# Kernel optimization log

Measured on AMD Instinct MI355X. Metric: run time of the kernel, lower is better.

## Reference

```python
import jax, jax.numpy as jnp
import numpy as np

B, H, W = 16, 32, 32
N = H * W
C_SEARCH, C_XCORR = 256, 64
C = C_SEARCH + C_XCORR          # phi_in_channels = gcn_in_channels
PHI_H = 64
GC_HID, GC_OUT = 128, 1
K_PTS = 48                       # keypoints per image
BN_EPS = 1e-5


def _build_coords_pair():
    # 8-neighbourhood pairs (distance^2 in {1,2}), exactly gen_8neigh_coords_pair
    idx = np.arange(N).reshape(H, W)
    ys, xs = np.meshgrid(np.arange(H), np.arange(W), indexing='ij')
    pairs8 = []
    for dy in (-1, 0, 1):
        for dx in (-1, 0, 1):
            if dy == 0 and dx == 0:
                continue
            ny, nx = ys + dy, xs + dx
            m = (ny >= 0) & (ny < H) & (nx >= 0) & (nx < W)
            pairs8.append(np.stack([idx[ys[m], xs[m]], idx[ny[m], nx[m]]], axis=1))
    pairs8 = np.concatenate(pairs8, 0)  # [7812, 2]
    # keypoint permutation pairs; keypoints on even coords -> disjoint from 8-neigh
    even = np.arange(0, H, 2)
    grid_idx = (even[:, None] * W + even[None, :]).reshape(-1)
    rng = np.random.default_rng(0)
    out = []
    for _ in range(B):
        kp = rng.choice(grid_idx, size=K_PTS, replace=False)
        a, b = np.meshgrid(kp, kp, indexing='ij')
        m = a != b
        kpairs = np.stack([a[m], b[m]], axis=1)  # K*(K-1) ordered pairs
        out.append(np.concatenate([kpairs, pairs8], 0))
    return np.stack(out, 0).astype(np.int32)  # [B, E, 2]


def setup_inputs() -> dict:
    key = jax.random.key(0)
    ks = jax.random.split(key, 10)
    u = lambda k, shape, s: jax.random.uniform(k, shape, jnp.float32, -s, s)
    inp = {
        'search_feature': jax.random.normal(ks[0], (B, C_SEARCH, H, W), jnp.float32),
        'xcorr_map': jax.random.normal(ks[1], (B, C_XCORR, H, W), jnp.float32),
        'coords_pair': jnp.asarray(_build_coords_pair()),
        # phi: Linear(C, PHI_H) + BN + ReLU, then Linear(PHI_H, 1) + Sigmoid
        'phi_w1': u(ks[2], (C, PHI_H), 1.0 / np.sqrt(C)),
        'phi_b1': u(ks[3], (PHI_H,), 1.0 / np.sqrt(C)),
        'bn_gamma': jnp.ones((PHI_H,), jnp.float32),
        'bn_beta': jnp.zeros((PHI_H,), jnp.float32),
        'phi_w2': u(ks[4], (PHI_H, 1), 1.0 / np.sqrt(PHI_H)),
        'phi_b2': u(ks[5], (1,), 1.0 / np.sqrt(PHI_H)),
        # GCN weights, torch init: uniform(-1/sqrt(out), 1/sqrt(out))
        'gc1_w': u(ks[6], (C, GC_HID), 1.0 / np.sqrt(GC_HID)),
        'gc2_w': u(ks[7], (GC_HID, GC_OUT), 1.0 / np.sqrt(GC_OUT)),
    }
    return inp


def reference(search_feature, xcorr_map, coords_pair, phi_w1, phi_b1,
              bn_gamma, bn_beta, phi_w2, phi_b2, gc1_w, gc2_w):
    # catted feature flattened: [B, C, N] (row-major h*W+w, matches torch view)
    feat = jnp.concatenate([search_feature, xcorr_map], axis=1).reshape(B, C, N)

    def per_image(f, pairs):  # f: [C, N], pairs: [E, 2]
        diff = jnp.abs(f[:, pairs[:, 0]] - f[:, pairs[:, 1]]).T  # [E, C]
        h = diff @ phi_w1 + phi_b1                                # [E, PHI_H]
        mu = jnp.mean(h, axis=0)
        var = jnp.var(h, axis=0)  # biased, as torch BN training mode
        h = (h - mu) / jnp.sqrt(var + BN_EPS) * bn_gamma + bn_beta
        h = jax.nn.relu(h)
        edge = jax.nn.sigmoid(h @ phi_w2 + phi_b2)[:, 0]          # [E]
        adj = jnp.zeros((N, N), jnp.float32).at[pairs[:, 0], pairs[:, 1]].set(edge)
        return adj

    adj = jax.vmap(per_image)(feat, coords_pair)  # [B, N, N]

    node_feat = feat.transpose(0, 2, 1)  # [B, N, C] (gcn_process_feat_xcorr=True)
    h = jax.nn.leaky_relu(jnp.einsum('bnm,bmd->bnd', adj, node_feat @ gc1_w), 0.2)
    mask = jax.nn.sigmoid(jnp.einsum('bnm,bmd->bnd', adj, h @ gc2_w))  # [B, N, 1]
    return mask[:, :, 0].reshape(B, 1, H, W)
```

## Files before the change

### kernel.cpp

```cpp
#include <hip/hip_runtime.h>
#include <hip/hip_bf16.h>
#include <hip/hip_fp16.h>

#define BB 16
#define NN 1024
#define CS 256
#define CX 64
#define CC 320
#define PH 64
#define GH 128
#define ELLW 64
#define NENG 7812
#define ROWP 324
#define RSTR 164
#define NKPH 1128
#define NGU  3906
#define NUD  5034

typedef __hip_bfloat16 bf16;
typedef __attribute__((ext_vector_type(8))) __bf16 bfrag;
typedef __attribute__((ext_vector_type(4))) float v4f;

__device__ __forceinline__ void tri_decode(int m, int& a, int& y) {
    float s = sqrtf((float)(9025 - 8 * m));
    int aa = (int)((95.0f - s) * 0.5f);
    if (aa > 0 && 47 * aa - (aa * (aa - 1)) / 2 > m) --aa;
    while (47 * (aa + 1) - ((aa + 1) * aa) / 2 <= m) ++aa;
    a = aa;
    y = aa + 1 + (m - (47 * aa - (aa * (aa - 1)) / 2));
}

__global__ __launch_bounds__(256) void k_prep_transpose(
    const float* __restrict__ search, const float* __restrict__ xcorr,
    float* __restrict__ featT,
    const float* __restrict__ w1, const float* __restrict__ gc1w,
    __bf16* __restrict__ whi, __bf16* __restrict__ wlo,
    __bf16* __restrict__ gwhi, __bf16* __restrict__ gwlo,
    int* __restrict__ cnt, float* __restrict__ Ssum, float* __restrict__ S2sum)
{
    __shared__ float tile[32][33];
    int blk = blockIdx.x;
    int tid = threadIdx.x;
    if (blk < BB * 320) {
        int b   = blk % BB;
        int rem = blk / BB;
        int ct  = rem >> 5;
        int ntl = rem & 31;
        int cl = tid >> 5, nl = tid & 31;
        const float* sb = search + (size_t)b * CS * NN;
        const float* xb = xcorr + (size_t)b * CX * NN;
        #pragma unroll
        for (int f = 0; f < 4; ++f) {
            int c = ct * 32 + cl + f * 8;
            int n = ntl * 32 + nl;
            float v = (c < CS) ? sb[(size_t)c * NN + n] : xb[(size_t)(c - CS) * NN + n];
            tile[cl + f * 8][nl] = v;
        }
        __syncthreads();
        #pragma unroll
        for (int f = 0; f < 4; ++f) {
            int nr = cl + f * 8;
            int cc = nl;
            featT[((size_t)b * NN + ntl * 32 + nr) * CC + ct * 32 + cc] = tile[cc][nr];
        }
    } else {
        int idx = (blk - BB * 320) * 256 + tid;
        if (idx < 10 * 4 * 64 * 8) {
            int j    = idx & 7;
            int lane = (idx >> 3) & 63;
            int nt   = (idx >> 9) & 3;
            int ks   = idx >> 11;
            int k = ks * 32 + (lane >> 4) * 8 + j;
            int n = nt * 16 + (lane & 15);
            float w = w1[k * PH + n];
            __bf16 h = (__bf16)w;
            whi[idx] = h;
            wlo[idx] = (__bf16)(w - (float)h);
        }
        if (idx < 10 * 8 * 64 * 8) {
            int j    = idx & 7;
            int lane = (idx >> 3) & 63;
            int nt   = (idx >> 9) & 7;
            int ks   = idx >> 12;
            int k = ks * 32 + (lane >> 4) * 8 + j;
            int n = nt * 16 + (lane & 15);
            float w = gc1w[k * GH + n];
            __bf16 h = (__bf16)w;
            gwhi[idx] = h;
            gwlo[idx] = (__bf16)(w - (float)h);
        }
        if (idx < BB * NN) cnt[idx] = 0;
        if (idx < BB * PH) { Ssum[idx] = 0.f; S2sum[idx] = 0.f; }
    }
}

__global__ __launch_bounds__(512, 1) void k_edge(
    const float* __restrict__ featT, const int* __restrict__ pairs,
    const uint4* __restrict__ wglob, const float* __restrict__ b1,
    bf16* __restrict__ hstore, float* __restrict__ Ssum,
    float* __restrict__ S2sum, int E, int EKP)
{
    __shared__ ushort Wsh[40960];
    __shared__ float RowsBuf[16000];
    __shared__ int kpn[48];

    int t = threadIdx.x;
    int wave = t >> 6, lane = t & 63;
    int q = lane >> 4, r = lane & 15;
    int b = blockIdx.x % BB;
    int s = blockIdx.x / BB;

    if (t < 48) kpn[t] = pairs[((size_t)b * E + t * 47) * 2];

    {
        uint4* dst = (uint4*)Wsh;
        #pragma unroll
        for (int k = 0; k < 10; ++k)
            dst[t + k * 512] = wglob[t + k * 512];
    }
    const bfrag* WH = (const bfrag*)Wsh;
    const bfrag* WL = (const bfrag*)(Wsh + 20480);

    float b1v[4];
    #pragma unroll
    for (int nt = 0; nt < 4; ++nt) b1v[nt] = b1[nt * 16 + r];
    float ps[4], ps2[4];
    #pragma unroll
    for (int nt = 0; nt < 4; ++nt) { ps[nt] = 0.f; ps2[nt] = 0.f; }

    const int dyT[4] = {-1,-1,-1, 0};
    const int dxT[4] = {-1, 0, 1,-1};
    const int pfT4[4] = {0, 961, 1953, 2914};

    int d = wave >> 1;
    int p = wave & 1;
    int dy = dyT[d], dx = dxT[d];
    int y0 = dy < 0 ? 1 : 0;
    int x0 = dx < 0 ? 1 : 0;
    int ww = (dx == 0) ? 32 : 31;
    int pfF = pfT4[d];
    int y = 2 * s + p;

    const float* rowI[2];
    const float* rowJ[2];
    #pragma unroll
    for (int mt = 0; mt < 2; ++mt) {
        int x  = (mt << 4) + r;
        int lr = 1 + p;
        int ni = lr * 32 + x;
        int xj = x + dx; xj = xj < 0 ? 0 : (xj > 31 ? 31 : xj);
        int nj = (lr + dy) * 32 + xj;
        rowI[mt] = &RowsBuf[ni * RSTR + q * 8];
        rowJ[mt] = &RowsBuf[nj * RSTR + q * 8];
    }

    v4f acc[2][4];
    #pragma unroll
    for (int mt = 0; mt < 2; ++mt)
        #pragma unroll
        for (int nt = 0; nt < 4; ++nt) acc[mt][nt] = (v4f)0.f;

    #pragma unroll
    for (int ph = 0; ph < 2; ++ph) {
        __syncthreads();
        const int ch0 = ph * 160;
        for (int uu = t; uu < 96 * 40; uu += 512) {
            int node = uu / 40, c4 = uu - node * 40;
            int gy = 2 * s - 1 + (node >> 5);
            if (gy >= 0) {
                int gn = gy * 32 + (node & 31);
                float4 v = *(const float4*)&featT[((size_t)b * NN + gn) * CC
                                                  + ch0 + c4 * 4];
                *(float4*)&RowsBuf[node * RSTR + c4 * 4] = v;
            }
        }
        __syncthreads();

        const int ksBeg = ph * 5;
        #pragma unroll
        for (int ks = ksBeg; ks < ksBeg + 5; ++ks) {
            int lc = ks * 32 - ch0;
            #pragma unroll
            for (int mt = 0; mt < 2; ++mt) {
                float4 fi0 = *(const float4*)(rowI[mt] + lc);
                float4 fi1 = *(const float4*)(rowI[mt] + lc + 4);
                float4 fj0 = *(const float4*)(rowJ[mt] + lc);
                float4 fj1 = *(const float4*)(rowJ[mt] + lc + 4);
                float df[8];
                df[0] = fabsf(fi0.x - fj0.x); df[1] = fabsf(fi0.y - fj0.y);
                df[2] = fabsf(fi0.z - fj0.z); df[3] = fabsf(fi0.w - fj0.w);
                df[4] = fabsf(fi1.x - fj1.x); df[5] = fabsf(fi1.y - fj1.y);
                df[6] = fabsf(fi1.z - fj1.z); df[7] = fabsf(fi1.w - fj1.w);

                bfrag ah, al;
                #pragma unroll
                for (int kk = 0; kk < 8; ++kk) {
                    __bf16 h = (__bf16)df[kk];
                    ah[kk] = h;
                    al[kk] = (__bf16)(df[kk] - (float)h);
                }
                #pragma unroll
                for (int nt = 0; nt < 4; ++nt) {
                    bfrag bh = WH[((ks * 4 + nt) << 6) + lane];
                    bfrag bl = WL[((ks * 4 + nt) << 6) + lane];
                    acc[mt][nt] = __builtin_amdgcn_mfma_f32_16x16x32_bf16(
                        ah, bh, acc[mt][nt], 0, 0, 0);
                    acc[mt][nt] = __builtin_amdgcn_mfma_f32_16x16x32_bf16(
                        ah, bl, acc[mt][nt], 0, 0, 0);
                    acc[mt][nt] = __builtin_amdgcn_mfma_f32_16x16x32_bf16(
                        al, bh, acc[mt][nt], 0, 0, 0);
                }
            }
        }
    }

    __syncthreads();
    {
        const float4* src = (const float4*)featT;
        #pragma unroll
        for (int k = 0; k < 8; ++k) {
            int idx = t + k * 512;
            if (idx < 48 * 80) {
                int slot = idx / 80, c4 = idx - slot * 80;
                float4 v = src[((size_t)b * NN + kpn[slot]) * 80 + c4];
                *(float4*)&RowsBuf[slot * ROWP + c4 * 4] = v;
            }
        }
    }

    #pragma unroll
    for (int mt = 0; mt < 2; ++mt) {
        #pragma unroll
        for (int reg = 0; reg < 4; ++reg) {
            int xi = (mt << 4) + q * 4 + reg;
            int y2 = y + dy, x2 = xi + dx;
            bool valid = ((unsigned)y2 < 32u) && ((unsigned)x2 < 32u);
            if (valid) {
                int e1 = EKP + pfF + (y - y0) * ww + (xi - x0);
                bf16* h1 = hstore + ((size_t)b * E + e1) * PH + r;
                #pragma unroll
                for (int nt = 0; nt < 4; ++nt) {
                    float v = acc[mt][nt][reg] + b1v[nt];
                    h1[nt * 16] = __float2bfloat16(v);
                    ps[nt] += v;
                    ps2[nt] = fmaf(v, v, ps2[nt]);
                }
            }
        }
    }

    __syncthreads();

    int u = s + 16 * wave;
    if (u < 71) {
        int mA = u * 16 + r;
        if (mA >= NKPH) mA = NKPH - 1;
        int aI, yI;
        tri_decode(mA, aI, yI);
        const float* rI = &RowsBuf[aI * ROWP + q * 8];
        const float* rJ = &RowsBuf[yI * ROWP + q * 8];

        v4f acc2[4];
        #pragma unroll
        for (int nt = 0; nt < 4; ++nt) acc2[nt] = (v4f)0.f;

        #pragma unroll
        for (int ks = 0; ks < 10; ++ks) {
            float4 fi0 = *(const float4*)(rI + ks * 32);
            float4 fi1 = *(const float4*)(rI + ks * 32 + 4);
            float4 fj0 = *(const float4*)(rJ + ks * 32);
            float4 fj1 = *(const float4*)(rJ + ks * 32 + 4);
            float df[8];
            df[0] = fabsf(fi0.x - fj0.x); df[1] = fabsf(fi0.y - fj0.y);
            df[2] = fabsf(fi0.z - fj0.z); df[3] = fabsf(fi0.w - fj0.w);
            df[4] = fabsf(fi1.x - fj1.x); df[5] = fabsf(fi1.y - fj1.y);
            df[6] = fabsf(fi1.z - fj1.z); df[7] = fabsf(fi1.w - fj1.w);

            bfrag ah, al;
            #pragma unroll
            for (int kk = 0; kk < 8; ++kk) {
                __bf16 h = (__bf16)df[kk];
                ah[kk] = h;
                al[kk] = (__bf16)(df[kk] - (float)h);
            }
            #pragma unroll
            for (int nt = 0; nt < 4; ++nt) {
                bfrag bh = WH[((ks * 4 + nt) << 6) + lane];
                bfrag bl = WL[((ks * 4 + nt) << 6) + lane];
                acc2[nt] = __builtin_amdgcn_mfma_f32_16x16x32_bf16(ah, bh, acc2[nt], 0, 0, 0);
                acc2[nt] = __builtin_amdgcn_mfma_f32_16x16x32_bf16(ah, bl, acc2[nt], 0, 0, 0);
                acc2[nt] = __builtin_amdgcn_mfma_f32_16x16x32_bf16(al, bh, acc2[nt], 0, 0, 0);
            }
        }

        #pragma unroll
        for (int reg = 0; reg < 4; ++reg) {
            int mC = u * 16 + q * 4 + reg;
            if (mC < NKPH) {
                int a, yk;
                tri_decode(mC, a, yk);
                int e1 = a * 47 + yk - 1;
                bf16* h1 = hstore + ((size_t)b * E + e1) * PH + r;
                #pragma unroll
                for (int nt = 0; nt < 4; ++nt) {
                    float v = acc2[nt][reg] + b1v[nt];
                    h1[nt * 16] = __float2bfloat16(v);
                    ps[nt] += v;
                    ps2[nt] = fmaf(v, v, ps2[nt]);
                }
            }
        }
    }

    __syncthreads();
    float* sS  = RowsBuf;
    float* sS2 = RowsBuf + PH;
    if (t < PH) { sS[t] = 0.f; sS2[t] = 0.f; }
    __syncthreads();
    #pragma unroll
    for (int nt = 0; nt < 4; ++nt) {
        float p1 = ps[nt]  + __shfl_xor(ps[nt], 16, 64);
        p1 += __shfl_xor(p1, 32, 64);
        float p2 = ps2[nt] + __shfl_xor(ps2[nt], 16, 64);
        p2 += __shfl_xor(p2, 32, 64);
        if (lane < 16) {
            atomicAdd(&sS[nt * 16 + r],  2.0f * p1);
            atomicAdd(&sS2[nt * 16 + r], 2.0f * p2);
        }
    }
    __syncthreads();
    if (t < PH) {
        atomicAdd(&Ssum[b * PH + t],  sS[t]);
        atomicAdd(&S2sum[b * PH + t], sS2[t]);
    }
}

__global__ __launch_bounds__(256, 2) void k_val_gc1(
    const float* __restrict__ featT, const __bf16* __restrict__ gwhi,
    const __bf16* __restrict__ gwlo, __half* __restrict__ g1,
    const bf16* __restrict__ hstore, const float* __restrict__ Ssum,
    const float* __restrict__ S2sum, const float* __restrict__ gamma,
    const float* __restrict__ beta, const float* __restrict__ w2,
    const float* __restrict__ b2, const int* __restrict__ pairs,
    int* __restrict__ cnt, int* __restrict__ ecol, float* __restrict__ eval_,
    int E, int EKP, int nGC)
{
    __shared__ ushort WG[40960];

    int t = threadIdx.x;
    if ((int)blockIdx.x < nGC) {
        int b = blockIdx.x % BB;
        int rem = blockIdx.x / BB;
        int half = rem & 1;
        int m0 = b * NN + (rem >> 1) * 64;

        {
            uint4* dst = (uint4*)WG;
            const uint4* sh = (const uint4*)gwhi;
            const uint4* sl = (const uint4*)gwlo;
            #pragma unroll
            for (int k = 0; k < 10; ++k) {
                int u = t + k * 256;
                int chunk = u >> 6, v = u & 63;
                int ks = chunk >> 2, ntp = chunk & 3;
                int src = (ks * 8 + half * 4 + ntp) * 64 + v;
                dst[u]        = sh[src];
                dst[2560 + u] = sl[src];
            }
        }

        int wave = t >> 6, lane = t & 63;
        int q = lane >> 4, r = lane & 15;
        const float* fp = featT + (size_t)(m0 + wave * 16 + r) * CC + q * 8;

        float fa[2][8];
        auto LOADA = [&](int ks, int buf) {
            const float4* p = (const float4*)(fp + ks * 32);
            *(float4*)&fa[buf][0] = p[0];
            *(float4*)&fa[buf][4] = p[1];
        };

        v4f acc[4];
        #pragma unroll
        for (int nt = 0; nt < 4; ++nt) acc[nt] = (v4f)0.f;

        LOADA(0, 0);
        __syncthreads();

        const bfrag* WGH = (const bfrag*)WG;
        const bfrag* WGL = (const bfrag*)(WG + 20480);

        #pragma unroll
        for (int ks = 0; ks < 10; ++ks) {
            int cur = ks & 1;
            if (ks < 9) LOADA(ks + 1, cur ^ 1);
            bfrag ah, al;
            #pragma unroll
            for (int kk = 0; kk < 8; ++kk) {
                float d = fa[cur][kk];
                __bf16 h = (__bf16)d;
                ah[kk] = h;
                al[kk] = (__bf16)(d - (float)h);
            }
            #pragma unroll
            for (int nt = 0; nt < 4; ++nt) {
                bfrag bh = WGH[((ks * 4 + nt) << 6) + lane];
                bfrag bl = WGL[((ks * 4 + nt) << 6) + lane];
                acc[nt] = __builtin_amdgcn_mfma_f32_16x16x32_bf16(ah, bh, acc[nt], 0, 0, 0);
                acc[nt] = __builtin_amdgcn_mfma_f32_16x16x32_bf16(ah, bl, acc[nt], 0, 0, 0);
                acc[nt] = __builtin_amdgcn_mfma_f32_16x16x32_bf16(al, bh, acc[nt], 0, 0, 0);
            }
        }
        #pragma unroll
        for (int nt = 0; nt < 4; ++nt) {
            #pragma unroll
            for (int reg = 0; reg < 4; ++reg) {
                int m = m0 + wave * 16 + q * 4 + reg;
                g1[(size_t)m * GH + (half * 4 + nt) * 16 + r] =
                    __float2half(acc[nt][reg]);
            }
        }
    } else {
        float* ca = (float*)WG;
        float* cb = ca + PH;
        int* kpl = (int*)(cb + PH);
        int blk = blockIdx.x - nGC;
        int b = blk % BB;
        int u = (blk / BB) * 256 + t;
        if (t < PH) {
            int l = t;
            float mu = Ssum[b * PH + l] / E;
            float var = S2sum[b * PH + l] / E - mu * mu;
            float A = rsqrtf(var + 1e-5f) * gamma[l];
            ca[l] = A;
            cb[l] = beta[l] - mu * A;
        }
        if (t < 48) kpl[t] = pairs[((size_t)b * E + t * 47) * 2];
        __syncthreads();
        if (u >= NUD) return;

        int i, j, hrow;
        if (u < NKPH) {
            int a, yk;
            tri_decode(u, a, yk);
            i = kpl[a]; j = kpl[yk];
            hrow = a * 47 + yk - 1;
        } else {
            int up = u - NKPH;
            int pf, ww, y0, x0, dy, dx;
            if (up < 961)       { pf = 0;    ww = 31; y0 = 1; x0 = 1; dy = -1; dx = -1; }
            else if (up < 1953) { pf = 961;  ww = 32; y0 = 1; x0 = 0; dy = -1; dx = 0;  }
            else if (up < 2914) { pf = 1953; ww = 31; y0 = 1; x0 = 0; dy = -1; dx = 1;  }
            else                { pf = 2914; ww = 31; y0 = 0; x0 = 1; dy = 0;  dx = -1; }
            int rel = up - pf;
            int yR = rel / ww, xC = rel - yR * ww;
            int yy = yR + y0, xi = xC + x0;
            i = yy * 32 + xi;
            j = (yy + dy) * 32 + (xi + dx);
            hrow = EKP + up;
        }

        const bfrag* hp = (const bfrag*)(hstore + ((size_t)b * E + hrow) * PH);
        float acc = 0.f;
        #pragma unroll
        for (int l8 = 0; l8 < 8; ++l8) {
            bfrag hv = hp[l8];
            #pragma unroll
            for (int c = 0; c < 8; ++c) {
                int l = l8 * 8 + c;
                float x = fmaf((float)hv[c], ca[l], cb[l]);
                x = x > 0.f ? x : 0.f;
                acc = fmaf(x, w2[l], acc);
            }
        }
        float edge = 1.f / (1.f + __expf(-(acc + b2[0])));
        int ri = b * NN + i;
        int rj = b * NN + j;
        int s1 = atomicAdd(&cnt[ri], 1);
        if (s1 < ELLW) {
            ecol[ri * ELLW + s1]  = j;
            eval_[ri * ELLW + s1] = edge;
        }
        int s2 = atomicAdd(&cnt[rj], 1);
        if (s2 < ELLW) {
            ecol[rj * ELLW + s2]  = i;
            eval_[rj * ELLW + s2] = edge;
        }
    }
}

__global__ __launch_bounds__(256) void k_spmm1(
    const __half* __restrict__ g1, const int* __restrict__ cnt,
    const int* __restrict__ ecol, const float* __restrict__ eval_,
    const float* __restrict__ w2g, float* __restrict__ g2)
{
    int tid = threadIdx.x & 63;
    int node = blockIdx.x * 4 + (threadIdx.x >> 6);
    int base = node & ~(NN - 1);
    float wa = w2g[2 * tid], wb = w2g[2 * tid + 1];
    int c = cnt[node];
    const int* ec = ecol + (size_t)node * ELLW;
    const float* ev = eval_ + (size_t)node * ELLW;
    const __half2* g1v = (const __half2*)g1;
    float aa = 0.f, ab = 0.f;
    int s = 0;
    for (; s + 4 <= c; s += 4) {
        int j0 = ec[s], j1 = ec[s + 1], j2 = ec[s + 2], j3 = ec[s + 3];
        float v0 = ev[s], v1 = ev[s + 1], v2 = ev[s + 2], v3 = ev[s + 3];
        __half2 u0 = g1v[((size_t)(base + j0)) * 64 + tid];
        __half2 u1 = g1v[((size_t)(base + j1)) * 64 + tid];
        __half2 u2 = g1v[((size_t)(base + j2)) * 64 + tid];
        __half2 u3 = g1v[((size_t)(base + j3)) * 64 + tid];
        aa = fmaf(v0, __low2float(u0), aa); ab = fmaf(v0, __high2float(u0), ab);
        aa = fmaf(v1, __low2float(u1), aa); ab = fmaf(v1, __high2float(u1), ab);
        aa = fmaf(v2, __low2float(u2), aa); ab = fmaf(v2, __high2float(u2), ab);
        aa = fmaf(v3, __low2float(u3), aa); ab = fmaf(v3, __high2float(u3), ab);
    }
    for (; s < c; ++s) {
        __half2 u = g1v[((size_t)(base + ec[s])) * 64 + tid];
        float v = ev[s];
        aa = fmaf(v, __low2float(u), aa); ab = fmaf(v, __high2float(u), ab);
    }
    float h1a = aa > 0.f ? aa : 0.2f * aa;
    float h1b = ab > 0.f ? ab : 0.2f * ab;
    float p = h1a * wa + h1b * wb;
    #pragma unroll
    for (int off = 32; off >= 1; off >>= 1) p += __shfl_down(p, off, 64);
    if (tid == 0) g2[node] = p;
}

__global__ __launch_bounds__(256) void k_spmm2(
    const float* __restrict__ g2, const int* __restrict__ cnt,
    const int* __restrict__ ecol, const float* __restrict__ eval_,
    float* __restrict__ out)
{
    int lane = threadIdx.x & 63;
    int node = blockIdx.x * 4 + (threadIdx.x >> 6);
    int base = node & ~(NN - 1);
    int c = cnt[node];
    float p = 0.f;
    if (lane < c) {
        int j = ecol[(size_t)node * ELLW + lane];
        p = eval_[(size_t)node * ELLW + lane] * g2[base + j];
    }
    #pragma unroll
    for (int off = 32; off >= 1; off >>= 1) p += __shfl_down(p, off, 64);
    if (lane == 0) out[node] = 1.f / (1.f + __expf(-p));
}

extern "C" void kernel_launch(void* const* d_in, const int* in_sizes, int n_in,
                              void* d_out, int out_size, void* d_ws, size_t ws_size,
                              hipStream_t stream)
{
    const float* search = (const float*)d_in[0];
    const float* xcorr  = (const float*)d_in[1];
    const int*   pairs  = (const int*)d_in[2];
    const float* w1     = (const float*)d_in[3];
    const float* b1     = (const float*)d_in[4];
    const float* gamma  = (const float*)d_in[5];
    const float* beta   = (const float*)d_in[6];
    const float* w2     = (const float*)d_in[7];
    const float* b2     = (const float*)d_in[8];
    const float* gc1w   = (const float*)d_in[9];
    const float* gc2w   = (const float*)d_in[10];
    float* out = (float*)d_out;

    int E   = in_sizes[2] / (BB * 2);
    int EKP = E - NENG;
    int nbU  = (NUD + 255) / 256;
    int nGC  = BB * 32;

    char* ws = (char*)d_ws;
    size_t off = 0;
    auto alloc = [&](size_t bytes) {
        size_t o = off;
        off += (bytes + 255) & ~(size_t)255;
        return o;
    };
    __bf16* whi   = (__bf16*)(ws + alloc(10 * 4 * 64 * 8 * 2));
    __bf16* wlo   = (__bf16*)(ws + alloc(10 * 4 * 64 * 8 * 2));
    __bf16* gwhi  = (__bf16*)(ws + alloc(10 * 8 * 64 * 8 * 2));
    __bf16* gwlo  = (__bf16*)(ws + alloc(10 * 8 * 64 * 8 * 2));
    float* featT  = (float*)(ws + alloc((size_t)BB * NN * CC * 4));
    bf16*  hstore = (bf16*)(ws + alloc((size_t)BB * E * PH * 2));
    float* Ssum   = (float*)(ws + alloc(BB * PH * 4));
    float* S2sum  = (float*)(ws + alloc(BB * PH * 4));
    int*   cnt    = (int*)(ws + alloc(BB * NN * 4));
    int*   ecol   = (int*)(ws + alloc((size_t)BB * NN * ELLW * 4));
    float* eval_  = (float*)(ws + alloc((size_t)BB * NN * ELLW * 4));
    __half* g1    = (__half*)(ws + alloc((size_t)BB * NN * GH * 2));
    float* g2     = (float*)(ws + alloc(BB * NN * 4));
    (void)ws_size; (void)n_in; (void)out_size;

    k_prep_transpose<<<dim3(BB * 320 + 160), dim3(256), 0, stream>>>(
        search, xcorr, featT, w1, gc1w, whi, wlo, gwhi, gwlo, cnt, Ssum, S2sum);
    k_edge<<<dim3(BB * 16), dim3(512), 0, stream>>>(featT, pairs,
                                                    (const uint4*)whi, b1,
                                                    hstore, Ssum, S2sum,
                                                    E, EKP);
    k_val_gc1<<<dim3(nGC + BB * nbU), dim3(256), 0, stream>>>(
        featT, gwhi, gwlo, g1, hstore, Ssum, S2sum, gamma, beta, w2, b2,
        pairs, cnt, ecol, eval_, E, EKP, nGC);
    k_spmm1<<<dim3(BB * NN / 4), dim3(256), 0, stream>>>(g1, cnt, ecol, eval_,
                                                         gc2w, g2);
    k_spmm2<<<dim3(BB * NN / 4), dim3(256), 0, stream>>>(g2, cnt, ecol, eval_, out);
}
```

Measured before the change: 148.2 us.

## Split edge kernel into one-row blocks and read weights directly from global

The edge-MLP kernel now launches twice as many blocks of 256 threads, each handling a single image row instead of two, with four waves covering the four neighbour directions. The per-block copy of the bf16 weight fragments into shared memory is removed, and fragments are loaded from global memory (through cache) during the MFMA loop. Together these cut LDS use so two blocks can share a CU and give more parallelism. The cost is reloading the 3-row halo per block, which is now redundant across neighbouring blocks, plus weight fetches that go to L1/L2 instead of LDS.

```diff
diff --git a/kernel.cpp b/kernel.cpp
--- a/kernel.cpp
+++ b/kernel.cpp
@@ -94,32 +94,25 @@
     }
 }
 
-__global__ __launch_bounds__(512, 1) void k_edge(
+__global__ __launch_bounds__(256, 2) void k_edge(
     const float* __restrict__ featT, const int* __restrict__ pairs,
-    const uint4* __restrict__ wglob, const float* __restrict__ b1,
+    const __bf16* __restrict__ wglob, const float* __restrict__ b1,
     bf16* __restrict__ hstore, float* __restrict__ Ssum,
     float* __restrict__ S2sum, int E, int EKP)
 {
-    __shared__ ushort Wsh[40960];
-    __shared__ float RowsBuf[16000];
+    __shared__ float RowsBuf[15552];
     __shared__ int kpn[48];
 
     int t = threadIdx.x;
     int wave = t >> 6, lane = t & 63;
     int q = lane >> 4, r = lane & 15;
     int b = blockIdx.x % BB;
-    int s = blockIdx.x / BB;
+    int y = blockIdx.x / BB;
 
     if (t < 48) kpn[t] = pairs[((size_t)b * E + t * 47) * 2];
 
-    {
-        uint4* dst = (uint4*)Wsh;
-        #pragma unroll
-        for (int k = 0; k < 10; ++k)
-            dst[t + k * 512] = wglob[t + k * 512];
-    }
-    const bfrag* WH = (const bfrag*)Wsh;
-    const bfrag* WL = (const bfrag*)(Wsh + 20480);
+    const bfrag* WH = (const bfrag*)wglob;
+    const bfrag* WL = WH + 2560;
 
     float b1v[4];
     #pragma unroll
@@ -132,24 +125,21 @@
     const int dxT[4] = {-1, 0, 1,-1};
     const int pfT4[4] = {0, 961, 1953, 2914};
 
-    int d = wave >> 1;
-    int p = wave & 1;
+    int d = wave;
     int dy = dyT[d], dx = dxT[d];
     int y0 = dy < 0 ? 1 : 0;
     int x0 = dx < 0 ? 1 : 0;
     int ww = (dx == 0) ? 32 : 31;
     int pfF = pfT4[d];
-    int y = 2 * s + p;
 
     const float* rowI[2];
     const float* rowJ[2];
     #pragma unroll
     for (int mt = 0; mt < 2; ++mt) {
         int x  = (mt << 4) + r;
-        int lr = 1 + p;
-        int ni = lr * 32 + x;
+        int ni = 32 + x;
         int xj = x + dx; xj = xj < 0 ? 0 : (xj > 31 ? 31 : xj);
-        int nj = (lr + dy) * 32 + xj;
+        int nj = (1 + dy) * 32 + xj;
         rowI[mt] = &RowsBuf[ni * RSTR + q * 8];
         rowJ[mt] = &RowsBuf[nj * RSTR + q * 8];
     }
@@ -164,9 +154,11 @@
     for (int ph = 0; ph < 2; ++ph) {
         __syncthreads();
         const int ch0 = ph * 160;
-        for (int uu = t; uu < 96 * 40; uu += 512) {
+        #pragma unroll
+        for (int k = 0; k < 10; ++k) {
+            int uu = t + k * 256;
             int node = uu / 40, c4 = uu - node * 40;
-            int gy = 2 * s - 1 + (node >> 5);
+            int gy = y - 1 + (node >> 5);
             if (gy >= 0) {
                 int gn = gy * 32 + (node & 31);
                 float4 v = *(const float4*)&featT[((size_t)b * NN + gn) * CC
@@ -218,13 +210,11 @@
     {
         const float4* src = (const float4*)featT;
         #pragma unroll
-        for (int k = 0; k < 8; ++k) {
-            int idx = t + k * 512;
-            if (idx < 48 * 80) {
-                int slot = idx / 80, c4 = idx - slot * 80;
-                float4 v = src[((size_t)b * NN + kpn[slot]) * 80 + c4];
-                *(float4*)&RowsBuf[slot * ROWP + c4 * 4] = v;
-            }
+        for (int k = 0; k < 15; ++k) {
+            int idx = t + k * 256;
+            int slot = idx / 80, c4 = idx - slot * 80;
+            float4 v = src[((size_t)b * NN + kpn[slot]) * 80 + c4];
+            *(float4*)&RowsBuf[slot * ROWP + c4 * 4] = v;
         }
     }
 
@@ -251,7 +241,7 @@
 
     __syncthreads();
 
-    int u = s + 16 * wave;
+    int u = y + 32 * wave;
     if (u < 71) {
         int mA = u * 16 + r;
         if (mA >= NKPH) mA = NKPH - 1;
@@ -594,8 +584,7 @@
 
     k_prep_transpose<<<dim3(BB * 320 + 160), dim3(256), 0, stream>>>(
         search, xcorr, featT, w1, gc1w, whi, wlo, gwhi, gwlo, cnt, Ssum, S2sum);
-    k_edge<<<dim3(BB * 16), dim3(512), 0, stream>>>(featT, pairs,
-                                                    (const uint4*)whi, b1,
+    k_edge<<<dim3(BB * 32), dim3(256), 0, stream>>>(featT, pairs, whi, b1,
                                                     hstore, Ssum, S2sum,
                                                     E, EKP);
     k_val_gc1<<<dim3(nGC + BB * nbU), dim3(256), 0, stream>>>(
```

Result: no change. 149.0 us (+0.5%).
